# Kernel tuning notes

Measured on AMD Instinct MI355X. Metric: run time of the kernel, lower is better.

## Reference

```python
import jax, jax.numpy as jnp
import numpy as np

FP8_MAX = 448.0
EPS = 1e-12


def setup_inputs() -> dict:
    key = jax.random.key(0)
    k1, k2 = jax.random.split(key)
    x = jax.random.normal(k1, (4, 2048, 4096), dtype=jnp.float32)
    # kaiming-uniform-like init scale for weight
    weight = jax.random.normal(k2, (4096, 4096), dtype=jnp.float32) * 0.02
    bias = jnp.zeros((4096,), dtype=jnp.float32)
    return {"x": x, "weight": weight, "bias": bias}


def reference(x, weight, bias):
    # per-tensor fake-quant of activations
    input_scale = jnp.maximum(jnp.max(jnp.abs(x)) / FP8_MAX, EPS)
    x_q = jnp.round(jnp.clip(x / input_scale, -FP8_MAX, FP8_MAX))
    # per-tensor fake-quant of weight
    weight_scale = jnp.maximum(jnp.max(jnp.abs(weight)) / FP8_MAX, EPS)
    weight_q = jnp.round(jnp.clip(weight / weight_scale, -FP8_MAX, FP8_MAX))
    # GEMM in quantized domain, then dequant rescale + bias
    out_q = jnp.einsum('bsi,oi->bso', x_q, weight_q)  # [B,S,out]
    out = (out_q * (input_scale * weight_scale)).astype(x.dtype) + bias
    return out
```

## Files before the change

### kernel.cpp

```cpp
#include <hip/hip_runtime.h>

#define FP8_MAX 448.0f
#define EPSF 1e-12f

#define BM 128
#define BN 128
#define BK 32

typedef __attribute__((ext_vector_type(8))) _Float16 half8;
typedef __attribute__((ext_vector_type(4))) float floatx4;

__device__ inline void async_copy16(const void* gp, void* lp) {
  __builtin_amdgcn_global_load_lds(
      (const __attribute__((address_space(1))) unsigned int*)gp,
      (__attribute__((address_space(3))) unsigned int*)lp,
      16, 0, 0);
}

__global__ void absmax_kernel(const float* __restrict__ in, int n4,
                              unsigned* __restrict__ out) {
  int tid = blockIdx.x * blockDim.x + threadIdx.x;
  int stride = gridDim.x * blockDim.x;
  const float4* in4 = (const float4*)in;
  float m = 0.f;
  for (int i = tid; i < n4; i += stride) {
    float4 v = in4[i];
    m = fmaxf(m, fmaxf(fmaxf(fabsf(v.x), fabsf(v.y)),
                       fmaxf(fabsf(v.z), fabsf(v.w))));
  }
  for (int off = 32; off > 0; off >>= 1)
    m = fmaxf(m, __shfl_down(m, off, 64));
  __shared__ float smax[4];
  int lane = threadIdx.x & 63, w = threadIdx.x >> 6;
  if (lane == 0) smax[w] = m;
  __syncthreads();
  if (threadIdx.x == 0) {
    float b = fmaxf(fmaxf(smax[0], smax[1]), fmaxf(smax[2], smax[3]));
    atomicMax(out, __float_as_uint(b));
  }
}

__global__ void quant_kernel(const float* __restrict__ in,
                             _Float16* __restrict__ out, int n8,
                             const unsigned* __restrict__ amax_bits) {
  const float scale = fmaxf(__uint_as_float(*amax_bits) / FP8_MAX, EPSF);
  int tid = blockIdx.x * blockDim.x + threadIdx.x;
  int stride = gridDim.x * blockDim.x;
  const float4* in4 = (const float4*)in;
  half8* out8 = (half8*)out;
  for (int i = tid; i < n8; i += stride) {
    float4 a = in4[2 * i], b = in4[2 * i + 1];
    half8 h;
    h[0] = (_Float16)rintf(fminf(fmaxf(a.x / scale, -FP8_MAX), FP8_MAX));
    h[1] = (_Float16)rintf(fminf(fmaxf(a.y / scale, -FP8_MAX), FP8_MAX));
    h[2] = (_Float16)rintf(fminf(fmaxf(a.z / scale, -FP8_MAX), FP8_MAX));
    h[3] = (_Float16)rintf(fminf(fmaxf(a.w / scale, -FP8_MAX), FP8_MAX));
    h[4] = (_Float16)rintf(fminf(fmaxf(b.x / scale, -FP8_MAX), FP8_MAX));
    h[5] = (_Float16)rintf(fminf(fmaxf(b.y / scale, -FP8_MAX), FP8_MAX));
    h[6] = (_Float16)rintf(fminf(fmaxf(b.z / scale, -FP8_MAX), FP8_MAX));
    h[7] = (_Float16)rintf(fminf(fmaxf(b.w / scale, -FP8_MAX), FP8_MAX));
    out8[i] = h;
  }
}

__global__ void gemm_q_kernel(const _Float16* __restrict__ A,
                              const _Float16* __restrict__ B,
                              const float* __restrict__ bias,
                              const unsigned* __restrict__ amax,
                              float* __restrict__ C,
                              int M, int N, int K) {
  __shared__ __align__(16) _Float16 As[BM * BK];
  __shared__ __align__(16) _Float16 Bs[BN * BK];

  const int tid = threadIdx.x;
  const int w = tid >> 6;
  const int lane = tid & 63;
  const int wr = w >> 1;
  const int wc = w & 1;
  const int bm = blockIdx.y;
  const int bn = blockIdx.x;

  const _Float16* Ab = A + (size_t)bm * BM * K;
  const _Float16* Bb = B + (size_t)bn * BN * K;

  const int srow = lane >> 2;
  const int scol = (lane & 3) * 8;

  floatx4 acc[4][4] = {};

  for (int k0 = 0; k0 < K; k0 += BK) {
#pragma unroll
    for (int c = 0; c < 2; ++c) {
      const int chunk = c * 4 + w;
      async_copy16(Ab + (size_t)(chunk * 16 + srow) * K + k0 + scol,
                   &As[chunk * 16 * BK]);
      async_copy16(Bb + (size_t)(chunk * 16 + srow) * K + k0 + scol,
                   &Bs[chunk * 16 * BK]);
    }
    __syncthreads();

    half8 af[4], bf[4];
#pragma unroll
    for (int i = 0; i < 4; ++i) {
      af[i] = *(const half8*)&As[(wr * 64 + i * 16 + (lane & 15)) * BK +
                                 (lane >> 4) * 8];
      bf[i] = *(const half8*)&Bs[(wc * 64 + i * 16 + (lane & 15)) * BK +
                                 (lane >> 4) * 8];
    }
#pragma unroll
    for (int mi = 0; mi < 4; ++mi)
#pragma unroll
      for (int ni = 0; ni < 4; ++ni)
        acc[mi][ni] = __builtin_amdgcn_mfma_f32_16x16x32_f16(
            af[mi], bf[ni], acc[mi][ni], 0, 0, 0);
    __syncthreads();
  }

  const float sx = fmaxf(__uint_as_float(amax[0]) / FP8_MAX, EPSF);
  const float sw = fmaxf(__uint_as_float(amax[1]) / FP8_MAX, EPSF);
  const float s = sx * sw;

  const int row0 = bm * BM + wr * 64 + (lane >> 4) * 4;
  const int col0 = bn * BN + wc * 64 + (lane & 15);

  float bv[4];
#pragma unroll
  for (int ni = 0; ni < 4; ++ni) bv[ni] = bias[col0 + ni * 16];

#pragma unroll
  for (int mi = 0; mi < 4; ++mi) {
#pragma unroll
    for (int ni = 0; ni < 4; ++ni) {
      const size_t base = (size_t)(row0 + mi * 16) * N + col0 + ni * 16;
#pragma unroll
      for (int r = 0; r < 4; ++r)
        C[base + (size_t)r * N] = acc[mi][ni][r] * s + bv[ni];
    }
  }
}

extern "C" void kernel_launch(void* const* d_in, const int* in_sizes, int n_in,
                              void* d_out, int out_size, void* d_ws,
                              size_t ws_size, hipStream_t stream) {
  const float* x = (const float*)d_in[0];
  const float* wgt = (const float*)d_in[1];
  const float* bias = (const float*)d_in[2];
  float* out = (float*)d_out;

  const int N = in_sizes[2];
  const int K = in_sizes[1] / N;
  const int M = in_sizes[0] / K;

  unsigned* amax = (unsigned*)d_ws;
  _Float16* xq = (_Float16*)((char*)d_ws + 256);
  _Float16* wq =
      (_Float16*)((char*)d_ws + 256 + (size_t)M * K * sizeof(_Float16));

  hipMemsetAsync(d_ws, 0, 8, stream);
  absmax_kernel<<<2048, 256, 0, stream>>>(x, M * K / 4, amax);
  absmax_kernel<<<1024, 256, 0, stream>>>(wgt, N * K / 4, amax + 1);
  quant_kernel<<<2048, 256, 0, stream>>>(x, xq, M * K / 8, amax);
  quant_kernel<<<1024, 256, 0, stream>>>(wgt, wq, N * K / 8, amax + 1);
  gemm_q_kernel<<<dim3(N / BN, M / BM), 256, 0, stream>>>(xq, wq, bias, amax,
                                                          out, M, N, K);
}
```

Measured before the change: 426.1 us.

## Restructure GEMM into 256x256 double-buffered pipeline with swizzled LDS and XCD remap

Replaces the 128x128x32 single-buffered GEMM with a 256x256x64 tile, 8 waves, and double-buffered LDS. Global-to-LDS async loads for the next K tiles are interleaved with four MFMA phases, with explicit waitcnt, barriers and setprio. LDS reads use an XOR swizzle to avoid bank conflicts, and block IDs are remapped across the 8 XCDs for L2 locality. The goal is to hide load latency and raise MFMA utilisation. The cost is higher register and LDS pressure plus fragile manual synchronisation.

New measurement: 408.4 us. -4.2%, faster.

```diff
diff --git a/kernel.cpp b/kernel.cpp
--- a/kernel.cpp
+++ b/kernel.cpp
@@ -3,9 +3,9 @@
 #define FP8_MAX 448.0f
 #define EPSF 1e-12f
 
-#define BM 128
-#define BN 128
-#define BK 32
+#define BM 256
+#define BN 256
+#define BK 64
 
 typedef __attribute__((ext_vector_type(8))) _Float16 half8;
 typedef __attribute__((ext_vector_type(4))) float floatx4;
@@ -63,78 +63,163 @@
   }
 }
 
-__global__ void gemm_q_kernel(const _Float16* __restrict__ A,
-                              const _Float16* __restrict__ B,
-                              const float* __restrict__ bias,
-                              const unsigned* __restrict__ amax,
-                              float* __restrict__ C,
-                              int M, int N, int K) {
-  __shared__ __align__(16) _Float16 As[BM * BK];
-  __shared__ __align__(16) _Float16 Bs[BN * BK];
+__global__ __launch_bounds__(512, 2) void gemm8_kernel(
+    const _Float16* __restrict__ A,
+    const _Float16* __restrict__ B,
+    const float* __restrict__ bias, const unsigned* __restrict__ amax,
+    float* __restrict__ C,
+    int M, int N, int K) {
+  __shared__ __align__(16) _Float16 As[2][BM * BK];
+  __shared__ __align__(16) _Float16 Bs[2][BN * BK];
 
   const int tid = threadIdx.x;
   const int w = tid >> 6;
   const int lane = tid & 63;
-  const int wr = w >> 1;
-  const int wc = w & 1;
-  const int bm = blockIdx.y;
-  const int bn = blockIdx.x;
+  const int wr = w >> 2;
+  const int wc = w & 3;
+
+  const int nwg = gridDim.x;
+  const int cpx = nwg >> 3;
+  const int swz = (blockIdx.x & 7) * cpx + (blockIdx.x >> 3);
+  const int nbn = N / BN;
+  const int bm = swz / nbn;
+  const int bn = swz % nbn;
 
   const _Float16* Ab = A + (size_t)bm * BM * K;
   const _Float16* Bb = B + (size_t)bn * BN * K;
 
-  const int srow = lane >> 2;
-  const int scol = (lane & 3) * 8;
-
-  floatx4 acc[4][4] = {};
-
-  for (int k0 = 0; k0 < K; k0 += BK) {
-#pragma unroll
-    for (int c = 0; c < 2; ++c) {
-      const int chunk = c * 4 + w;
-      async_copy16(Ab + (size_t)(chunk * 16 + srow) * K + k0 + scol,
-                   &As[chunk * 16 * BK]);
-      async_copy16(Bb + (size_t)(chunk * 16 + srow) * K + k0 + scol,
-                   &Bs[chunk * 16 * BK]);
+  const int srow8 = w * 8 + (lane >> 3);
+  const int gd8 = ((lane & 7) ^ ((lane >> 3) & 7)) * 8;
+  const _Float16* Ag = Ab + (size_t)srow8 * K + gd8;
+  const _Float16* Bg = Bb + (size_t)srow8 * K + gd8;
+
+  auto stageA = [&](int kt, int h) {
+#pragma unroll
+    for (int r = 0; r < 2; ++r)
+      async_copy16(Ag + (size_t)(h * 128 + r * 64) * K + kt * BK,
+                   (void*)&As[kt & 1][(h * 128 + r * 64 + w * 8) * BK]);
+  };
+  auto stageB = [&](int kt, int h) {
+#pragma unroll
+    for (int r = 0; r < 2; ++r)
+      async_copy16(Bg + (size_t)(h * 128 + r * 64) * K + kt * BK,
+                   (void*)&Bs[kt & 1][(h * 128 + r * 64 + w * 8) * BK]);
+  };
+
+  const int lr = lane & 15;
+  const int hi = lane >> 4;
+  const int aoff = (wr * 128 + lr) * BK;
+  const int boff = (wc * 64 + lr) * BK;
+  const int g0 = ((hi) ^ (lr & 7)) * 8;
+  const int g1 = ((4 + hi) ^ (lr & 7)) * 8;
+
+  floatx4 acc[8][4] = {};
+  const int nt = K / BK;
+
+  stageA(0, 0); stageA(0, 1); stageB(0, 0); stageB(0, 1);
+  stageA(1, 0); stageA(1, 1);
+  asm volatile("s_waitcnt vmcnt(4)" ::: "memory");
+  __builtin_amdgcn_s_barrier();
+
+  for (int t = 0; t < nt; ++t) {
+    const int b = t & 1;
+    const _Float16* Asb = &As[b][0];
+    const _Float16* Bsb = &Bs[b][0];
+    half8 a_lo0[4], a_hi0[4], a_lo1[4], a_hi1[4], bf0[4], bf1[4];
+
+#pragma unroll
+    for (int m = 0; m < 4; ++m)
+      a_lo0[m] = *(const half8*)&Asb[aoff + m * 16 * BK + g0];
+#pragma unroll
+    for (int n = 0; n < 4; ++n)
+      bf0[n] = *(const half8*)&Bsb[boff + n * 16 * BK + g0];
+    if (t + 1 < nt) stageB(t + 1, 0);
+    __builtin_amdgcn_s_barrier();
+    asm volatile("s_waitcnt lgkmcnt(0)");
+    __builtin_amdgcn_s_setprio(1);
+#pragma unroll
+    for (int m = 0; m < 4; ++m)
+#pragma unroll
+      for (int n = 0; n < 4; ++n)
+        acc[m][n] = __builtin_amdgcn_mfma_f32_16x16x32_f16(
+            a_lo0[m], bf0[n], acc[m][n], 0, 0, 0);
+    __builtin_amdgcn_s_setprio(0);
+    __builtin_amdgcn_s_barrier();
+
+#pragma unroll
+    for (int m = 0; m < 4; ++m)
+      a_hi0[m] = *(const half8*)&Asb[aoff + (64 + m * 16) * BK + g0];
+#pragma unroll
+    for (int n = 0; n < 4; ++n)
+      bf1[n] = *(const half8*)&Bsb[boff + n * 16 * BK + g1];
+    if (t + 1 < nt) stageB(t + 1, 1);
+    __builtin_amdgcn_s_barrier();
+    asm volatile("s_waitcnt lgkmcnt(0)");
+    __builtin_amdgcn_s_setprio(1);
+#pragma unroll
+    for (int m = 0; m < 4; ++m)
+#pragma unroll
+      for (int n = 0; n < 4; ++n)
+        acc[4 + m][n] = __builtin_amdgcn_mfma_f32_16x16x32_f16(
+            a_hi0[m], bf0[n], acc[4 + m][n], 0, 0, 0);
+    __builtin_amdgcn_s_setprio(0);
+    __builtin_amdgcn_s_barrier();
+
+#pragma unroll
+    for (int m = 0; m < 4; ++m)
+      a_lo1[m] = *(const half8*)&Asb[aoff + m * 16 * BK + g1];
+#pragma unroll
+    for (int m = 0; m < 4; ++m)
+      a_hi1[m] = *(const half8*)&Asb[aoff + (64 + m * 16) * BK + g1];
+    __builtin_amdgcn_s_barrier();
+    asm volatile("s_waitcnt lgkmcnt(0)");
+    __builtin_amdgcn_s_setprio(1);
+#pragma unroll
+    for (int m = 0; m < 4; ++m)
+#pragma unroll
+      for (int n = 0; n < 4; ++n)
+        acc[m][n] = __builtin_amdgcn_mfma_f32_16x16x32_f16(
+            a_lo1[m], bf1[n], acc[m][n], 0, 0, 0);
+    __builtin_amdgcn_s_setprio(0);
+    __builtin_amdgcn_s_barrier();
+
+    __builtin_amdgcn_sched_barrier(0);
+    if (t + 2 < nt) { stageA(t + 2, 0); stageA(t + 2, 1); }
+    __builtin_amdgcn_s_barrier();
+    __builtin_amdgcn_s_setprio(1);
+#pragma unroll
+    for (int m = 0; m < 4; ++m)
+#pragma unroll
+      for (int n = 0; n < 4; ++n)
+        acc[4 + m][n] = __builtin_amdgcn_mfma_f32_16x16x32_f16(
+            a_hi1[m], bf1[n], acc[4 + m][n], 0, 0, 0);
+    __builtin_amdgcn_s_setprio(0);
+    if (t + 2 < nt) {
+      asm volatile("s_waitcnt vmcnt(4)" ::: "memory");
+    } else {
+      asm volatile("s_waitcnt vmcnt(0)" ::: "memory");
     }
-    __syncthreads();
-
-    half8 af[4], bf[4];
-#pragma unroll
-    for (int i = 0; i < 4; ++i) {
-      af[i] = *(const half8*)&As[(wr * 64 + i * 16 + (lane & 15)) * BK +
-                                 (lane >> 4) * 8];
-      bf[i] = *(const half8*)&Bs[(wc * 64 + i * 16 + (lane & 15)) * BK +
-                                 (lane >> 4) * 8];
-    }
-#pragma unroll
-    for (int mi = 0; mi < 4; ++mi)
-#pragma unroll
-      for (int ni = 0; ni < 4; ++ni)
-        acc[mi][ni] = __builtin_amdgcn_mfma_f32_16x16x32_f16(
-            af[mi], bf[ni], acc[mi][ni], 0, 0, 0);
-    __syncthreads();
+    __builtin_amdgcn_s_barrier();
   }
 
   const float sx = fmaxf(__uint_as_float(amax[0]) / FP8_MAX, EPSF);
   const float sw = fmaxf(__uint_as_float(amax[1]) / FP8_MAX, EPSF);
   const float s = sx * sw;
 
-  const int row0 = bm * BM + wr * 64 + (lane >> 4) * 4;
-  const int col0 = bn * BN + wc * 64 + (lane & 15);
-
+  const int row0 = bm * BM + wr * 128 + hi * 4;
+  const int col0 = bn * BN + wc * 64 + lr;
   float bv[4];
 #pragma unroll
-  for (int ni = 0; ni < 4; ++ni) bv[ni] = bias[col0 + ni * 16];
-
-#pragma unroll
-  for (int mi = 0; mi < 4; ++mi) {
-#pragma unroll
-    for (int ni = 0; ni < 4; ++ni) {
-      const size_t base = (size_t)(row0 + mi * 16) * N + col0 + ni * 16;
+  for (int n = 0; n < 4; ++n) bv[n] = bias[col0 + n * 16];
+
+#pragma unroll
+  for (int m = 0; m < 8; ++m) {
+#pragma unroll
+    for (int n = 0; n < 4; ++n) {
+      const size_t base = (size_t)(row0 + m * 16) * N + col0 + n * 16;
 #pragma unroll
       for (int r = 0; r < 4; ++r)
-        C[base + (size_t)r * N] = acc[mi][ni][r] * s + bv[ni];
+        C[base + (size_t)r * N] = acc[m][n][r] * s + bv[n];
     }
   }
 }
@@ -161,6 +246,7 @@
   absmax_kernel<<<1024, 256, 0, stream>>>(wgt, N * K / 4, amax + 1);
   quant_kernel<<<2048, 256, 0, stream>>>(x, xq, M * K / 8, amax);
   quant_kernel<<<1024, 256, 0, stream>>>(wgt, wq, N * K / 8, amax + 1);
-  gemm_q_kernel<<<dim3(N / BN, M / BM), 256, 0, stream>>>(xq, wq, bias, amax,
-                                                          out, M, N, K);
-}
+
+  gemm8_kernel<<<dim3((M / BM) * (N / BN)), 512, 0, stream>>>(
+      xq, wq, bias, amax, out, M, N, K);
+}
```
